# Optimization experiments

Hardware: AMD Instinct MI355X
Metric: run time of the kernel (lower is better)

## Reference

```python
import jax, jax.numpy as jnp
import numpy as np

N = 4096          # batch size
D = 1024          # embedding dim
NUM_INSTANCES = 8 # samples per class (balanced batch, required by the original resize logic)
ALPHA = 20.0
MARGIN = 0.5


def setup_inputs() -> dict:
    key = jax.random.key(0)
    inputs = jax.random.normal(key, (N, D), dtype=jnp.float32)
    # balanced targets: each class appears exactly NUM_INSTANCES times
    targets = (jnp.arange(N, dtype=jnp.int32) // NUM_INSTANCES).astype(jnp.int32)
    return {"inputs": inputs, "targets": targets}


def reference(inputs, targets):
    n = inputs.shape[0]
    k_pos = NUM_INSTANCES - 1          # positives per row (excl. self)
    k_neg = n - NUM_INSTANCES          # negatives per row

    # L2 normalize rows, cosine similarity matrix [n, n]
    x = inputs / jnp.linalg.norm(inputs, axis=1, keepdims=True)
    sim = x @ x.T

    same = targets[:, None] == targets[None, :]
    eye = jnp.eye(n, dtype=bool)
    pos_mask = same & ~eye             # positives, diag removed
    neg_mask = ~same                   # negatives

    INF = jnp.float32(1e9)
    # per-row sorted positive / negative sims (ascending); fixed-size slices
    pos_sorted = jnp.sort(jnp.where(pos_mask, sim, INF), axis=1)[:, :k_pos]   # [n, k_pos]
    neg_sorted = jnp.sort(jnp.where(neg_mask, sim, INF), axis=1)[:, :k_neg]   # [n, k_neg]

    # base = max(max(sim) - 0.1, margin + 0.2)
    base = jnp.maximum(jnp.max(sim) - 0.1, MARGIN + 0.2)

    # dynamic selection expressed as masks over fixed-size sorted arrays
    neg_keep = neg_sorted > (pos_sorted[:, :1] - 0.05)   # negatives above min positive - 0.05
    pos_keep = pos_sorted < base                          # positives below base

    pos_elem = jnp.log1p(jnp.exp(-2.0 * (pos_sorted - MARGIN)))   # [n, k_pos]
    neg_elem = jnp.log1p(jnp.exp(ALPHA * (neg_sorted - MARGIN)))  # [n, k_neg]

    pos_cnt = pos_keep.sum(axis=1)
    neg_cnt = neg_keep.sum(axis=1)

    pos_mean = (pos_elem * pos_keep).sum(axis=1) / jnp.maximum(pos_cnt, 1).astype(sim.dtype)
    neg_mean = (neg_elem * neg_keep).sum(axis=1) / jnp.maximum(neg_cnt, 1).astype(sim.dtype)

    # fallbacks: empty pos set -> smallest positive; empty neg set -> largest negative
    pos_loss = jnp.where(pos_cnt > 0, pos_mean, pos_elem[:, 0])
    neg_loss = jnp.where(neg_cnt > 0, neg_mean, neg_elem[:, -1])

    return jnp.mean(pos_loss + neg_loss)   # sum over rows / n
```

## Files before the change

### kernel.cpp

```cpp
#include <hip/hip_runtime.h>
#include <hip/hip_bf16.h>
#include <hip/hip_fp8.h>
#include <math.h>

#define N 4096
#define D 1024
#define NINST 8
#define NGROUP (N / NINST)
#define ALPHA 20.0f
#define MARGIN 0.5f
#define NB 64
#define NTILE (NB * (NB + 1) / 2)

typedef __attribute__((ext_vector_type(4))) float f32x4;

__device__ __forceinline__ unsigned fkey(float f) {
    int b = __float_as_int(f);
    return (b >= 0) ? ((unsigned)b | 0x80000000u) : ~(unsigned)b;
}
__device__ __forceinline__ float fdec(unsigned u) {
    int b = (u & 0x80000000u) ? (int)(u ^ 0x80000000u) : ~(int)u;
    return __int_as_float(b);
}

__device__ __forceinline__ float softplus(float x) {
    float z = __expf(-fabsf(x));
    return fmaxf(x, 0.0f) + __logf(1.0f + z);
}

__global__ __launch_bounds__(256) void k_normpos(const float* __restrict__ in,
                                                 unsigned long* __restrict__ xn8,
                                                 float* __restrict__ pos_sims,
                                                 float* __restrict__ min_pos,
                                                 unsigned* __restrict__ gmax,
                                                 float* __restrict__ accum,
                                                 unsigned* __restrict__ cnt) {
    __shared__ float4 srows4[8 * 257];
    __shared__ float spart[8][4];
    __shared__ float sinv[8];
    __shared__ float sg[8][8];

    int g = blockIdx.x;
    int t = threadIdx.x;
    int lane = t & 63, wid = t >> 6;

    if (g == 0) {
        if (t == 0) { *gmax = 0u; *cnt = 0u; }
        if (t < 32) accum[t] = 0.f;
    }

    const float4* in4 = (const float4*)in;
    #pragma unroll
    for (int i = 0; i < 8; ++i) {
        float4 v = in4[(size_t)g * 2048 + i * 256 + t];
        srows4[i * 257 + t] = v;
        float ss = v.x * v.x + v.y * v.y + v.z * v.z + v.w * v.w;
        #pragma unroll
        for (int off = 1; off < 64; off <<= 1) ss += __shfl_xor(ss, off);
        if (lane == 0) spart[i][wid] = ss;
    }
    __syncthreads();
    if (t < 8) sinv[t] = rsqrtf(spart[t][0] + spart[t][1] + spart[t][2] + spart[t][3]);
    __syncthreads();

    {
        int i_row = t & 7;
        int oct  = (t >> 3) & 3;
        int k0b  = t >> 5;
        int lane16 = i_row + (g & 1) * 8;
        size_t blk = (size_t)(g >> 1);
        float inv = sinv[i_row];
        #pragma unroll
        for (int j = 0; j < 4; ++j) {
            int k0 = k0b + j * 8;
            float4 v0 = srows4[i_row * 257 + k0 * 8 + oct * 2];
            float4 v1 = srows4[i_row * 257 + k0 * 8 + oct * 2 + 1];
            union { unsigned char c[8]; unsigned long u64; } o;
            o.c[0] = __hip_fp8_e4m3(v0.x * inv).__x;
            o.c[1] = __hip_fp8_e4m3(v0.y * inv).__x;
            o.c[2] = __hip_fp8_e4m3(v0.z * inv).__x;
            o.c[3] = __hip_fp8_e4m3(v0.w * inv).__x;
            o.c[4] = __hip_fp8_e4m3(v1.x * inv).__x;
            o.c[5] = __hip_fp8_e4m3(v1.y * inv).__x;
            o.c[6] = __hip_fp8_e4m3(v1.z * inv).__x;
            o.c[7] = __hip_fp8_e4m3(v1.w * inv).__x;
            xn8[blk * 2048 + (size_t)k0 * 64 + (lane16 + oct * 16)] = o.u64;
        }
    }

    int pair = t >> 2, a = pair >> 3, b = pair & 7, slice = t & 3;
    const float4* pa = srows4 + a * 257 + slice * 64;
    const float4* pb = srows4 + b * 257 + slice * 64;
    float s = 0.f;
    #pragma unroll 8
    for (int i = 0; i < 64; ++i) {
        float4 x = pa[i], y = pb[i];
        s += x.x * y.x + x.y * y.y + x.z * y.z + x.w * y.w;
    }
    s += __shfl_xor(s, 1);
    s += __shfl_xor(s, 2);
    if (slice == 0) sg[a][b] = s * sinv[a] * sinv[b];
    __syncthreads();
    if (t < 8) {
        float mn = 1e30f;
        int idx = 0;
        #pragma unroll
        for (int b2 = 0; b2 < 8; ++b2) {
            if (b2 == t) continue;
            float v = sg[t][b2];
            mn = fminf(mn, v);
            pos_sims[(size_t)(g * 8 + t) * 8 + idx] = v;
            ++idx;
        }
        min_pos[g * 8 + t] = mn;
    }
}

__global__ __launch_bounds__(64, 2) void k_neg(const unsigned long* __restrict__ xn8,
                                               const float* __restrict__ min_pos,
                                               float* __restrict__ sum_part,
                                               int* __restrict__ cnt_part,
                                               float* __restrict__ max_part,
                                               unsigned* __restrict__ gmax) {
    int bid = blockIdx.x;
    int rt = 0, rem = bid;
    while (rem >= NB - rt) { rem -= NB - rt; ++rt; }
    int ct = rt + rem;
    bool diag = (rt == ct);

    int R0 = rt * 64, C0 = ct * 64;
    int l = threadIdx.x;
    int lrow = l & 15;
    int kgrp = l >> 4;

    float mA = min_pos[R0 + l];
    float mB = min_pos[C0 + l];

    const unsigned long* fA = xn8 + (size_t)(R0 >> 4) * 2048 + l;
    const unsigned long* fB = xn8 + (size_t)(C0 >> 4) * 2048 + l;

    f32x4 zero = {0.f, 0.f, 0.f, 0.f};
    f32x4 acc[4][4];
    #pragma unroll
    for (int m = 0; m < 4; ++m)
        #pragma unroll
        for (int n = 0; n < 4; ++n) acc[m][n] = zero;

    long a0[4], b0[4], a1[4], b1[4], a2[4], b2[4], a3[4], b3[4];

    #define LOADF(A, B, k0)                                           \
        do {                                                          \
            _Pragma("unroll")                                         \
            for (int m = 0; m < 4; ++m) {                             \
                A[m] = (long)fA[(size_t)m * 2048 + (k0) * 64];        \
                B[m] = (long)fB[(size_t)m * 2048 + (k0) * 64];        \
            }                                                         \
        } while (0)

    #define MFMAS(A, B)                                                       \
        do {                                                                  \
            _Pragma("unroll")                                                 \
            for (int m = 0; m < 4; ++m)                                       \
                _Pragma("unroll")                                             \
                for (int n = 0; n < 4; ++n)                                   \
                    acc[m][n] = __builtin_amdgcn_mfma_f32_16x16x32_fp8_fp8(   \
                        A[m], B[n], acc[m][n], 0, 0, 0);                      \
        } while (0)

    LOADF(a0, b0, 0);
    LOADF(a1, b1, 1);
    LOADF(a2, b2, 2);
    LOADF(a3, b3, 3);
    for (int it = 0; it <= 24; it += 4) {
        MFMAS(a0, b0); LOADF(a0, b0, it + 4);
        MFMAS(a1, b1); LOADF(a1, b1, it + 5);
        MFMAS(a2, b2); LOADF(a2, b2, it + 6);
        MFMAS(a3, b3); LOADF(a3, b3, it + 7);
    }
    MFMAS(a0, b0);
    MFMAS(a1, b1);
    MFMAS(a2, b2);
    MFMAS(a3, b3);
    #undef LOADF
    #undef MFMAS

    float allmax = -1e30f;

    float thB[4];
    #pragma unroll
    for (int n = 0; n < 4; ++n) thB[n] = __shfl(mB, n * 16 + lrow) - 0.05f;

    float colS[4] = {0.f, 0.f, 0.f, 0.f};
    float colM[4] = {-1e30f, -1e30f, -1e30f, -1e30f};
    int   colC[4] = {0, 0, 0, 0};

    #pragma unroll
    for (int m = 0; m < 4; ++m) {
        #pragma unroll
        for (int reg = 0; reg < 4; ++reg) {
            int lr = m * 16 + kgrp * 4 + reg;
            int grow = R0 + lr;
            float th = __shfl(mA, lr) - 0.05f;
            int gi = grow >> 3;
            float rs = 0.f, rm = -1e30f;
            int rc = 0;
            #pragma unroll
            for (int n = 0; n < 4; ++n) {
                int gcol = C0 + n * 16 + lrow;
                float s = acc[m][n][reg];
                allmax = fmaxf(allmax, s);
                if ((gcol >> 3) != gi) {
                    float e = softplus(ALPHA * (s - MARGIN));
                    rm = fmaxf(rm, s);
                    if (s > th) { rs += e; rc += 1; }
                    if (!diag) {
                        colM[n] = fmaxf(colM[n], s);
                        if (s > thB[n]) { colS[n] += e; colC[n] += 1; }
                    }
                }
            }
            #pragma unroll
            for (int off = 1; off < 16; off <<= 1) {
                rs += __shfl_xor(rs, off);
                rc += __shfl_xor(rc, off);
                rm = fmaxf(rm, __shfl_xor(rm, off));
            }
            if (lrow == 0) {
                sum_part[(size_t)grow * 64 + ct] = rs;
                cnt_part[(size_t)grow * 64 + ct] = rc;
                max_part[(size_t)grow * 64 + ct] = rm;
            }
        }
    }

    if (!diag) {
        #pragma unroll
        for (int n = 0; n < 4; ++n) {
            float cs = colS[n], cm = colM[n];
            int cc = colC[n];
            cs += __shfl_xor(cs, 16); cs += __shfl_xor(cs, 32);
            cc += __shfl_xor(cc, 16); cc += __shfl_xor(cc, 32);
            cm = fmaxf(cm, __shfl_xor(cm, 16));
            cm = fmaxf(cm, __shfl_xor(cm, 32));
            if (kgrp == 0) {
                int gcol = C0 + n * 16 + lrow;
                sum_part[(size_t)gcol * 64 + rt] = cs;
                cnt_part[(size_t)gcol * 64 + rt] = cc;
                max_part[(size_t)gcol * 64 + rt] = cm;
            }
        }
    }

    #pragma unroll
    for (int off = 1; off < 64; off <<= 1) allmax = fmaxf(allmax, __shfl_xor(allmax, off));
    if (l == 0) atomicMax(gmax, fkey(allmax));
}

__global__ __launch_bounds__(256) void k_rowfinal(const float* __restrict__ sum_part,
                                                  const int* __restrict__ cnt_part,
                                                  const float* __restrict__ max_part,
                                                  const float* __restrict__ pos_sims,
                                                  const float* __restrict__ min_pos,
                                                  const unsigned* __restrict__ gmax,
                                                  float* __restrict__ accum,
                                                  unsigned* __restrict__ cnt,
                                                  float* __restrict__ out) {
    __shared__ float sloss[4];
    int row = blockIdx.x * 4 + (threadIdx.x >> 6);
    int lane = threadIdx.x & 63;
    float ns = sum_part[(size_t)row * 64 + lane];
    int nc = cnt_part[(size_t)row * 64 + lane];
    float nm = max_part[(size_t)row * 64 + lane];
    #pragma unroll
    for (int off = 1; off < 64; off <<= 1) {
        ns += __shfl_xor(ns, off);
        nc += __shfl_xor(nc, off);
        nm = fmaxf(nm, __shfl_xor(nm, off));
    }
    if (lane == 0) {
        float base = fmaxf(fdec(*gmax) - 0.1f, MARGIN + 0.2f);
        float neg_loss = (nc > 0) ? ns / (float)nc : softplus(ALPHA * (nm - MARGIN));
        float ps = 0.f;
        int pcnt = 0;
        float mn = min_pos[row];
        #pragma unroll
        for (int i = 0; i < NINST - 1; ++i) {
            float s = pos_sims[(size_t)row * 8 + i];
            if (s < base) { ps += softplus(-2.0f * (s - MARGIN)); pcnt++; }
        }
        float pos_loss = (pcnt > 0) ? ps / (float)pcnt : softplus(-2.0f * (mn - MARGIN));
        sloss[threadIdx.x >> 6] = pos_loss + neg_loss;
    }
    __syncthreads();
    if (threadIdx.x == 0) {
        float bs = sloss[0] + sloss[1] + sloss[2] + sloss[3];
        atomicAdd(&accum[blockIdx.x & 31], bs);
        __threadfence();
        unsigned old = atomicAdd(cnt, 1u);
        if (old == gridDim.x - 1) {
            __threadfence();
            float tot = 0.f;
            for (int j = 0; j < 32; ++j) tot += atomicAdd(&accum[j], 0.0f);
            out[0] = tot / (float)N;
        }
    }
}

extern "C" void kernel_launch(void* const* d_in, const int* in_sizes, int n_in,
                              void* d_out, int out_size, void* d_ws, size_t ws_size,
                              hipStream_t stream) {
    const float* in = (const float*)d_in[0];
    float* out = (float*)d_out;

    char* ws = (char*)d_ws;
    unsigned long* xn8 = (unsigned long*)(ws);
    float*   min_pos  = (float*)(ws + 8388608 + 16384);
    float*   pos_sims = (float*)(ws + 8388608 + 32768);
    float*   sum_part = (float*)(ws + 8388608 + 32768 + 131072);
    float*   max_part = (float*)(ws + 8388608 + 32768 + 131072 + 1048576);
    int*     cnt_part = (int*)  (ws + 8388608 + 32768 + 131072 + 2097152);
    unsigned* gmax    = (unsigned*)(ws + 8388608 + 32768 + 131072 + 3145728);
    float*   accum    = (float*)(ws + 8388608 + 32768 + 131072 + 3145728 + 128);
    unsigned* cnt     = (unsigned*)(ws + 8388608 + 32768 + 131072 + 3145728 + 256);

    k_normpos<<<NGROUP, 256, 0, stream>>>(in, xn8, pos_sims, min_pos, gmax, accum, cnt);
    k_neg<<<NTILE, 64, 0, stream>>>(xn8, min_pos, sum_part, cnt_part, max_part, gmax);
    k_rowfinal<<<N / 4, 256, 0, stream>>>(sum_part, cnt_part, max_part, pos_sims, min_pos,
                                          gmax, accum, cnt, out);
}
```

Before: 118.8 us.

## Stage fp8 operand tiles through LDS via global_load_lds with 4-deep ring

```diff
diff --git a/kernel.cpp b/kernel.cpp
--- a/kernel.cpp
+++ b/kernel.cpp
@@ -26,6 +26,12 @@
 __device__ __forceinline__ float softplus(float x) {
     float z = __expf(-fabsf(x));
     return fmaxf(x, 0.0f) + __logf(1.0f + z);
+}
+
+__device__ __forceinline__ void gld16(const void* g, void* l) {
+    __builtin_amdgcn_global_load_lds(
+        (const __attribute__((address_space(1))) void*)g,
+        (__attribute__((address_space(3))) void*)l, 16, 0, 0);
 }
 
 __global__ __launch_bounds__(256) void k_normpos(const float* __restrict__ in,
@@ -67,8 +73,8 @@
         int i_row = t & 7;
         int oct  = (t >> 3) & 3;
         int k0b  = t >> 5;
-        int lane16 = i_row + (g & 1) * 8;
-        size_t blk = (size_t)(g >> 1);
+        size_t base = (size_t)(g >> 3) * 8192 + (size_t)((g >> 1) & 3) * 64
+                    + (size_t)(oct * 16 + (g & 1) * 8 + i_row);
         float inv = sinv[i_row];
         #pragma unroll
         for (int j = 0; j < 4; ++j) {
@@ -84,7 +90,7 @@
             o.c[5] = __hip_fp8_e4m3(v1.y * inv).__x;
             o.c[6] = __hip_fp8_e4m3(v1.z * inv).__x;
             o.c[7] = __hip_fp8_e4m3(v1.w * inv).__x;
-            xn8[blk * 2048 + (size_t)k0 * 64 + (lane16 + oct * 16)] = o.u64;
+            xn8[base + (size_t)k0 * 256] = o.u64;
         }
     }
 
@@ -122,6 +128,8 @@
                                                int* __restrict__ cnt_part,
                                                float* __restrict__ max_part,
                                                unsigned* __restrict__ gmax) {
+    __shared__ char sbuf[4][4096];
+
     int bid = blockIdx.x;
     int rt = 0, rem = bid;
     while (rem >= NB - rt) { rem -= NB - rt; ++rt; }
@@ -135,9 +143,22 @@
 
     float mA = min_pos[R0 + l];
     float mB = min_pos[C0 + l];
-
-    const unsigned long* fA = xn8 + (size_t)(R0 >> 4) * 2048 + l;
-    const unsigned long* fB = xn8 + (size_t)(C0 >> 4) * 2048 + l;
+    asm volatile("s_waitcnt vmcnt(0)" ::: "memory");
+
+    const char* xb = (const char*)xn8;
+    const char* gA = xb + (size_t)rt * 65536 + (size_t)l * 16;
+    const char* gB = xb + (size_t)ct * 65536 + (size_t)l * 16;
+
+    #define STAGE(s)                                                    \
+        do {                                                            \
+            char* d_ = sbuf[(s) & 3];                                   \
+            gld16(gA + (size_t)(s) * 2048,        d_);                  \
+            gld16(gA + (size_t)(s) * 2048 + 1024, d_ + 1024);           \
+            gld16(gB + (size_t)(s) * 2048,        d_ + 2048);           \
+            gld16(gB + (size_t)(s) * 2048 + 1024, d_ + 3072);           \
+        } while (0)
+
+    STAGE(0); STAGE(1); STAGE(2); STAGE(3);
 
     f32x4 zero = {0.f, 0.f, 0.f, 0.f};
     f32x4 acc[4][4];
@@ -146,43 +167,30 @@
         #pragma unroll
         for (int n = 0; n < 4; ++n) acc[m][n] = zero;
 
-    long a0[4], b0[4], a1[4], b1[4], a2[4], b2[4], a3[4], b3[4];
-
-    #define LOADF(A, B, k0)                                           \
-        do {                                                          \
-            _Pragma("unroll")                                         \
-            for (int m = 0; m < 4; ++m) {                             \
-                A[m] = (long)fA[(size_t)m * 2048 + (k0) * 64];        \
-                B[m] = (long)fB[(size_t)m * 2048 + (k0) * 64];        \
-            }                                                         \
-        } while (0)
-
-    #define MFMAS(A, B)                                                       \
-        do {                                                                  \
-            _Pragma("unroll")                                                 \
-            for (int m = 0; m < 4; ++m)                                       \
-                _Pragma("unroll")                                             \
-                for (int n = 0; n < 4; ++n)                                   \
-                    acc[m][n] = __builtin_amdgcn_mfma_f32_16x16x32_fp8_fp8(   \
-                        A[m], B[n], acc[m][n], 0, 0, 0);                      \
-        } while (0)
-
-    LOADF(a0, b0, 0);
-    LOADF(a1, b1, 1);
-    LOADF(a2, b2, 2);
-    LOADF(a3, b3, 3);
-    for (int it = 0; it <= 24; it += 4) {
-        MFMAS(a0, b0); LOADF(a0, b0, it + 4);
-        MFMAS(a1, b1); LOADF(a1, b1, it + 5);
-        MFMAS(a2, b2); LOADF(a2, b2, it + 6);
-        MFMAS(a3, b3); LOADF(a3, b3, it + 7);
-    }
-    MFMAS(a0, b0);
-    MFMAS(a1, b1);
-    MFMAS(a2, b2);
-    MFMAS(a3, b3);
-    #undef LOADF
-    #undef MFMAS
+    for (int it = 0; it < 32; ++it) {
+        if (it <= 28)      asm volatile("s_waitcnt vmcnt(12)" ::: "memory");
+        else if (it == 29) asm volatile("s_waitcnt vmcnt(8)"  ::: "memory");
+        else if (it == 30) asm volatile("s_waitcnt vmcnt(4)"  ::: "memory");
+        else               asm volatile("s_waitcnt vmcnt(0)"  ::: "memory");
+
+        const char* buf = sbuf[it & 3];
+        long a[4], b[4];
+        #pragma unroll
+        for (int m = 0; m < 4; ++m) {
+            a[m] = *(const long*)(buf + m * 512 + l * 8);
+            b[m] = *(const long*)(buf + 2048 + m * 512 + l * 8);
+        }
+        asm volatile("s_waitcnt lgkmcnt(0)" ::: "memory");
+        if (it <= 27) STAGE(it + 4);
+
+        #pragma unroll
+        for (int m = 0; m < 4; ++m)
+            #pragma unroll
+            for (int n = 0; n < 4; ++n)
+                acc[m][n] = __builtin_amdgcn_mfma_f32_16x16x32_fp8_fp8(
+                    a[m], b[n], acc[m][n], 0, 0, 0);
+    }
+    #undef STAGE
 
     float allmax = -1e30f;
 
```

Measured after the change: 104.0 us. 12.4% less time.
